# Kernel tuning notes

Hardware: AMD Instinct MI355X
Metric: run time of the kernel (lower is better)

The kernel has to match this reference:

```python
import jax, jax.numpy as jnp
import numpy as np

M, K, N = 32, 8192, 8192      # tokens, infeatures, outfeatures
GROUP = 128                   # quantization group size along K
PACK = 8                      # 32 bits / 4 bits per value


def _dequant(qweight, scales):
    """Unpack int4 nibbles (packed 8-per-int32 along K) and apply per-group
    symmetric dequant: w = (q - 8) * scale, matching Marlin's fused dequant."""
    kp, n = qweight.shape  # (K//8, N)
    shifts = (4 * jnp.arange(PACK, dtype=jnp.int32))[None, :, None]
    q = ((qweight[:, None, :] >> shifts) & 15)          # (K//8, 8, N)
    q = q.reshape(kp * PACK, n).astype(jnp.float32)     # (K, N)
    groups = scales.shape[0]
    gsz = (kp * PACK) // groups
    w = (q.reshape(groups, gsz, n) - 8.0) * scales[:, None, :]
    return w.reshape(kp * PACK, n)                      # (K, N) fp


def setup_inputs() -> dict:
    key = jax.random.key(0)
    kA, kQ, kS, kB = jax.random.split(key, 4)
    A = jax.random.normal(kA, (M, K), jnp.float32)
    # draw raw 4-bit codes then pack 8 of them into each int32 along K
    q4 = jax.random.randint(kQ, (K, N), 0, 16, jnp.int32)
    shifts = (4 * jnp.arange(PACK, dtype=jnp.int32))[None, :, None]
    qweight = jnp.sum(q4.reshape(K // PACK, PACK, N) << shifts, axis=1).astype(jnp.int32)
    scales = jax.random.uniform(kS, (K // GROUP, N), jnp.float32, 0.005, 0.02)
    bias = jax.random.normal(kB, (N,), jnp.float32) * 0.01
    return {"A": A, "qweight": qweight, "scales": scales, "bias": bias}


def reference(A, qweight, scales, bias):
    # Marlin mul(A, B, C, s) computes C = A @ dequant(B, s); then + bias
    W = _dequant(qweight, scales)          # (K, N)
    return A @ W + bias                    # (M, N)
```

## Files before the change

kernel.cpp:

```cpp
#include <hip/hip_runtime.h>
#include <hip/hip_bf16.h>
#include <stdint.h>

#define M_DIM 32
#define K_DIM 8192
#define N_DIM 8192
#define NGROUPS 64
#define KSPLIT 8
#define KPART (K_DIM / KSPLIT)
#define GPART (NGROUPS / KSPLIT)
#define BN 256

#define QSTRIDE 264
#define ASTRIDE 68
#define SSTRIDE 260

typedef __attribute__((ext_vector_type(8))) short short8;
typedef __attribute__((ext_vector_type(4))) float floatx4;

__global__ void marlin_prep_kernel(const float* __restrict__ A,
                                   uint16_t* __restrict__ Abf,
                                   float* __restrict__ R) {
    const int m = blockIdx.x;
    const int qtr = blockIdx.y;
    const int t = threadIdx.x;
    const int octet = qtr * 256 + t;
    const int k0 = octet * 8;

    const float* a = A + m * K_DIM + k0;
    uint16_t b[8];
    float sum = 0.f;
#pragma unroll
    for (int j = 0; j < 8; j++) {
        union { __hip_bfloat16 h; uint16_t u; } cv;
        cv.h = __float2bfloat16(a[j]);
        b[j] = cv.u;
        sum += __bfloat162float(cv.h);
    }
    uint32_t w0 = (uint32_t)b[0] | ((uint32_t)b[4] << 16);
    uint32_t w1 = (uint32_t)b[1] | ((uint32_t)b[5] << 16);
    uint32_t w2 = (uint32_t)b[2] | ((uint32_t)b[6] << 16);
    uint32_t w3 = (uint32_t)b[3] | ((uint32_t)b[7] << 16);
    *(uint4*)(Abf + (size_t)m * K_DIM + k0) = make_uint4(w0, w1, w2, w3);

#pragma unroll
    for (int off = 1; off < 16; off <<= 1) sum += __shfl_xor(sum, off, 16);
    if ((t & 15) == 0) R[m * NGROUPS + qtr * 16 + (t >> 4)] = sum;
}

__global__ __launch_bounds__(512, 2) void
MarlinQuantLinear_68556267979256_kernel(const int* __restrict__ qw,
                                        const float* __restrict__ scales,
                                        const uint16_t* __restrict__ Abf,
                                        const float* __restrict__ R,
                                        float* __restrict__ parts) {
    __shared__ uint32_t qbuf[2][16 * QSTRIDE];
    __shared__ uint32_t abuf[2][32 * ASTRIDE];
    __shared__ float    s_lds[GPART * SSTRIDE];
    __shared__ float    r_lds[32 * 9];

    const int bz = blockIdx.x;
    const int bx = blockIdx.y;
    const int nbase = bx * BN;
    const int gbase = bz * GPART;

    const int tid = threadIdx.x;
    const int w = tid >> 6;
    const int lane = tid & 63;
    const int quad = lane >> 4;
    const int l16 = lane & 15;
    const int mtile = w & 1;
    const int ntile = w >> 1;

    const int qr = tid >> 5;
    const int qc = (tid & 31) * 4;
    const int* qsrc = qw + (size_t)(bz * 128 + qr) * N_DIM + nbase + qc;
    const int ar = tid >> 4;
    const int ac = (tid & 15) * 4;
    const uint32_t* asrc = (const uint32_t*)Abf + (size_t)ar * (K_DIM / 2)
                           + bz * (KPART / 2) + ac;

    uint4 q0 = *(const uint4*)qsrc;
    uint4 q1 = *(const uint4*)(qsrc + 128);
    uint4 a0 = *(const uint4*)asrc;

    {
        const int sg = tid >> 6, scc = (tid & 63) * 4;
        const float4 sv = *(const float4*)(scales + (size_t)(gbase + sg) * N_DIM
                                           + nbase + scc);
        *(float4*)&s_lds[sg * SSTRIDE + scc] = sv;
    }
    if (tid < 256) {
        const int mm = tid >> 3, gg = tid & 7;
        r_lds[mm * 9 + gg] = 136.0f * R[mm * NGROUPS + gbase + gg];
    }

    floatx4 C[4] = {{0.f, 0.f, 0.f, 0.f}, {0.f, 0.f, 0.f, 0.f},
                    {0.f, 0.f, 0.f, 0.f}, {0.f, 0.f, 0.f, 0.f}};

#pragma unroll
    for (int g = 0; g < GPART; g++) {
        *(uint4*)&qbuf[g & 1][qr * QSTRIDE + qc] = q0;
        *(uint4*)&qbuf[g & 1][qr * QSTRIDE + qc + 128] = q1;
        *(uint4*)&abuf[g & 1][ar * ASTRIDE + ac] = a0;
        asm volatile("s_waitcnt lgkmcnt(0)" ::: "memory");
        __builtin_amdgcn_s_barrier();

        if (g + 1 < GPART) {
            q0 = *(const uint4*)(qsrc + (size_t)(g + 1) * 16 * N_DIM);
            q1 = *(const uint4*)(qsrc + (size_t)(g + 1) * 16 * N_DIM + 128);
            a0 = *(const uint4*)(asrc + (g + 1) * 64);
        }

        floatx4 accg[4] = {{0.f, 0.f, 0.f, 0.f}, {0.f, 0.f, 0.f, 0.f},
                           {0.f, 0.f, 0.f, 0.f}, {0.f, 0.f, 0.f, 0.f}};
#pragma unroll
        for (int t = 0; t < 4; t++) {
            const short8 fa = *(const short8*)
                &abuf[g & 1][(mtile * 16 + l16) * ASTRIDE + t * 16 + quad * 4];
#pragma unroll
            for (int f = 0; f < 4; f++) {
                const uint32_t q =
                    qbuf[g & 1][(t * 4 + quad) * QSTRIDE + ntile * 64 + f * 16 + l16];
                union { uint32_t u[4]; short8 v; } fb;
                fb.u[0] = ( q        & 0x000F000Fu) | 0x43004300u;
                fb.u[1] = ((q >> 4)  & 0x000F000Fu) | 0x43004300u;
                fb.u[2] = ((q >> 8)  & 0x000F000Fu) | 0x43004300u;
                fb.u[3] = ((q >> 12) & 0x000F000Fu) | 0x43004300u;
                accg[f] = __builtin_amdgcn_mfma_f32_16x16x32_bf16(fa, fb.v, accg[f], 0, 0, 0);
            }
        }
#pragma unroll
        for (int f = 0; f < 4; f++) {
            const float sv = s_lds[g * SSTRIDE + ntile * 64 + f * 16 + l16];
#pragma unroll
            for (int r = 0; r < 4; r++) {
                const float tval = accg[f][r] - r_lds[(mtile * 16 + quad * 4 + r) * 9 + g];
                C[f][r] = fmaf(sv, tval, C[f][r]);
            }
        }
    }

#pragma unroll
    for (int f = 0; f < 4; f++) {
        const int ncol = nbase + ntile * 64 + f * 16 + l16;
        float* pp = parts + ((size_t)bz * M_DIM + mtile * 16 + quad * 4) * N_DIM + ncol;
#pragma unroll
        for (int r = 0; r < 4; r++) pp[r * N_DIM] = C[f][r];
    }
}

__global__ __launch_bounds__(256) void
marlin_reduce_kernel(const float* __restrict__ parts,
                     const float* __restrict__ bias,
                     float* __restrict__ out) {
    const int idx = blockIdx.x * 256 + threadIdx.x;
    const int c4 = idx & (N_DIM / 4 - 1);
    const float4* p4 = (const float4*)parts;
    float4 acc = *(const float4*)(bias + c4 * 4);
#pragma unroll
    for (int bz = 0; bz < KSPLIT; bz++) {
        const float4 v = p4[(size_t)bz * (M_DIM * N_DIM / 4) + idx];
        acc.x += v.x; acc.y += v.y; acc.z += v.z; acc.w += v.w;
    }
    ((float4*)out)[idx] = acc;
}

extern "C" void kernel_launch(void* const* d_in, const int* in_sizes, int n_in,
                              void* d_out, int out_size, void* d_ws, size_t ws_size,
                              hipStream_t stream) {
    const float* A      = (const float*)d_in[0];
    const int*   qw     = (const int*)d_in[1];
    const float* scales = (const float*)d_in[2];
    const float* bias   = (const float*)d_in[3];
    float* out = (float*)d_out;

    uint16_t* Abf   = (uint16_t*)d_ws;
    float*    R     = (float*)((char*)d_ws + (size_t)M_DIM * K_DIM * 2);
    float*    parts = (float*)((char*)d_ws + (1 << 20));

    marlin_prep_kernel<<<dim3(M_DIM, 4), 256, 0, stream>>>(A, Abf, R);
    MarlinQuantLinear_68556267979256_kernel<<<dim3(KSPLIT, N_DIM / BN), 512, 0, stream>>>(
        qw, scales, Abf, R, parts);
    marlin_reduce_kernel<<<dim3((M_DIM * N_DIM / 4) / 256), 256, 0, stream>>>(
        parts, bias, out);
}
```

Measured before the change: 91.39 us.

## Replace split-K partial buffer and reduce kernel with atomic accumulation into output

The prep kernel now also zeroes the output. The main GEMM kernel atomically adds its split-K partial sums, plus bias from the first K slice, straight into the output. This removes the third launch and the write and re-read of the 8 MB partials buffer. In exchange it issues many scalar float atomics (8-way contention per element) and makes the summation order nondeterministic.

```diff
diff --git a/kernel.cpp b/kernel.cpp
--- a/kernel.cpp
+++ b/kernel.cpp
@@ -20,12 +20,20 @@
 
 __global__ void marlin_prep_kernel(const float* __restrict__ A,
                                    uint16_t* __restrict__ Abf,
-                                   float* __restrict__ R) {
+                                   float* __restrict__ R,
+                                   float4* __restrict__ out4) {
     const int m = blockIdx.x;
     const int qtr = blockIdx.y;
     const int t = threadIdx.x;
     const int octet = qtr * 256 + t;
     const int k0 = octet * 8;
+
+    {
+        const int gtid = (qtr * 32 + m) * 256 + t;
+        const float4 z = make_float4(0.f, 0.f, 0.f, 0.f);
+        out4[gtid * 2] = z;
+        out4[gtid * 2 + 1] = z;
+    }
 
     const float* a = A + m * K_DIM + k0;
     uint16_t b[8];
@@ -53,7 +61,8 @@
                                         const float* __restrict__ scales,
                                         const uint16_t* __restrict__ Abf,
                                         const float* __restrict__ R,
-                                        float* __restrict__ parts) {
+                                        const float* __restrict__ bias,
+                                        float* __restrict__ out) {
     __shared__ uint32_t qbuf[2][16 * QSTRIDE];
     __shared__ uint32_t abuf[2][32 * ASTRIDE];
     __shared__ float    s_lds[GPART * SSTRIDE];
@@ -144,26 +153,13 @@
 #pragma unroll
     for (int f = 0; f < 4; f++) {
         const int ncol = nbase + ntile * 64 + f * 16 + l16;
-        float* pp = parts + ((size_t)bz * M_DIM + mtile * 16 + quad * 4) * N_DIM + ncol;
+        const float bv = (bz == 0) ? bias[ncol] : 0.0f;
 #pragma unroll
-        for (int r = 0; r < 4; r++) pp[r * N_DIM] = C[f][r];
+        for (int r = 0; r < 4; r++) {
+            const int m = mtile * 16 + quad * 4 + r;
+            atomicAdd(&out[(size_t)m * N_DIM + ncol], C[f][r] + bv);
+        }
     }
-}
-
-__global__ __launch_bounds__(256) void
-marlin_reduce_kernel(const float* __restrict__ parts,
-                     const float* __restrict__ bias,
-                     float* __restrict__ out) {
-    const int idx = blockIdx.x * 256 + threadIdx.x;
-    const int c4 = idx & (N_DIM / 4 - 1);
-    const float4* p4 = (const float4*)parts;
-    float4 acc = *(const float4*)(bias + c4 * 4);
-#pragma unroll
-    for (int bz = 0; bz < KSPLIT; bz++) {
-        const float4 v = p4[(size_t)bz * (M_DIM * N_DIM / 4) + idx];
-        acc.x += v.x; acc.y += v.y; acc.z += v.z; acc.w += v.w;
-    }
-    ((float4*)out)[idx] = acc;
 }
 
 extern "C" void kernel_launch(void* const* d_in, const int* in_sizes, int n_in,
@@ -175,13 +171,10 @@
     const float* bias   = (const float*)d_in[3];
     float* out = (float*)d_out;
 
-    uint16_t* Abf   = (uint16_t*)d_ws;
-    float*    R     = (float*)((char*)d_ws + (size_t)M_DIM * K_DIM * 2);
-    float*    parts = (float*)((char*)d_ws + (1 << 20));
+    uint16_t* Abf = (uint16_t*)d_ws;
+    float*    R   = (float*)((char*)d_ws + (size_t)M_DIM * K_DIM * 2);
 
-    marlin_prep_kernel<<<dim3(M_DIM, 4), 256, 0, stream>>>(A, Abf, R);
+    marlin_prep_kernel<<<dim3(M_DIM, 4), 256, 0, stream>>>(A, Abf, R, (float4*)out);
     MarlinQuantLinear_68556267979256_kernel<<<dim3(KSPLIT, N_DIM / BN), 512, 0, stream>>>(
-        qw, scales, Abf, R, parts);
-    marlin_reduce_kernel<<<dim3((M_DIM * N_DIM / 4) / 256), 256, 0, stream>>>(
-        parts, bias, out);
+        qw, scales, Abf, R, bias, out);
 }
```

Measured after the change: 95.76 us. 1.05x slower.
